# Kernel optimization log

Hardware: AMD Instinct MI355X
Metric: run time of the kernel (lower is better)

## Reference

```python
import jax, jax.numpy as jnp
import numpy as np

EPS = 1e-5
EXTEND_SCOPE = 1.0

def conv2d(x, w, b, pad):
    out = jax.lax.conv_general_dilated(x, w, (1, 1), [(pad, pad), (pad, pad)],
                                       dimension_numbers=('NCHW', 'OIHW', 'NCHW'))
    return out + b[None, :, None, None]

def group_norm(x, groups, gamma, beta):
    B, C, H, W = x.shape
    xg = x.reshape(B, groups, -1)
    mu = xg.mean(-1, keepdims=True)
    var = xg.var(-1, keepdims=True)
    xn = ((xg - mu) * jax.lax.rsqrt(var + EPS)).reshape(B, C, H, W)
    return xn * gamma[None, :, None, None] + beta[None, :, None, None]

def bilinear_sample(feat, y, x):
    # feat [B,C,H,W]; y,x pixel coords [B,Ho,Wo]; zeros padding, align_corners=True
    B, C, H, W = feat.shape
    flat = feat.reshape(B, C, H * W)
    y0 = jnp.floor(y); x0 = jnp.floor(x)
    wy = (y - y0)[:, None]; wx = (x - x0)[:, None]  # [B,1,Ho,Wo]
    y0i = y0.astype(jnp.int32); x0i = x0.astype(jnp.int32)
    Ho, Wo = y.shape[1], y.shape[2]
    def gather(yi, xi):
        valid = ((yi >= 0) & (yi < H) & (xi >= 0) & (xi < W)).astype(feat.dtype)[:, None]
        idx = (jnp.clip(yi, 0, H - 1) * W + jnp.clip(xi, 0, W - 1)).reshape(B, -1)
        g = jax.vmap(lambda f, i: f[:, i])(flat, idx).reshape(B, C, Ho, Wo)
        return g * valid
    g00 = gather(y0i, x0i)
    g01 = gather(y0i, x0i + 1)
    g10 = gather(y0i + 1, x0i)
    g11 = gather(y0i + 1, x0i + 1)
    return g00 * (1 - wy) * (1 - wx) + g01 * (1 - wy) * wx + g10 * wy * (1 - wx) + g11 * wy * wx

def setup_inputs() -> dict:
    key = jax.random.key(0)
    ks = jax.random.split(key, 4)
    B, C, H, W, K, O = 4, 64, 128, 128, 9, 64
    return {
        'x': jax.random.normal(ks[0], (B, C, H, W), jnp.float32),
        'w_off': jax.random.normal(ks[1], (K, C, 3, 3), jnp.float32) * 0.05,
        'b_off': jnp.zeros((K,), jnp.float32),
        'w_theta': jax.random.normal(ks[2], (K, C, 5, 5), jnp.float32) * 0.05,
        'b_theta': jnp.zeros((K,), jnp.float32),
        'gn_off_g': jnp.ones((K,), jnp.float32),
        'gn_off_b': jnp.zeros((K,), jnp.float32),
        'gn_th_g': jnp.ones((K,), jnp.float32),
        'gn_th_b': jnp.zeros((K,), jnp.float32),
        'w_strip': jax.random.normal(ks[3], (O, C, K, 1), jnp.float32) * 0.05,
        'b_strip': jnp.zeros((O,), jnp.float32),
        'gn_out_g': jnp.ones((O,), jnp.float32),
        'gn_out_b': jnp.zeros((O,), jnp.float32),
    }

def reference(x, w_off, b_off, w_theta, b_theta, gn_off_g, gn_off_b,
              gn_th_g, gn_th_b, w_strip, b_strip, gn_out_g, gn_out_b):
    B, C, H, W = x.shape
    K = w_off.shape[0]
    center = K // 2
    off = jnp.tanh(group_norm(conv2d(x, w_off, b_off, 1), 3, gn_off_g, gn_off_b))       # [B,K,H,W]
    th = jnp.arctan(group_norm(conv2d(x, w_theta, b_theta, 2), 3, gn_th_g, gn_th_b))    # [B,K,H,W]
    k = jnp.arange(K)
    s = (k - center).astype(x.dtype)[None, :, None, None]   # signed kernel offset
    m = center + jnp.abs(k - center)                        # mirror index (uses theta/offset at center+|i|)
    th_m = th[:, m]; off_m = off[:, m]                      # [B,K,H,W]
    is_center = (k == center)[None, :, None, None]
    y_off = jnp.where(is_center, 0.0, s * jnp.tan(th_m) + off_m * jnp.cos(th_m))
    x_off = jnp.where(is_center, 0.0, s - jnp.sin(th_m) * off_m)
    y_new = jnp.arange(H, dtype=x.dtype)[None, None, :, None] + s + EXTEND_SCOPE * y_off
    x_new = jnp.arange(W, dtype=x.dtype)[None, None, None, :] + s + EXTEND_SCOPE * x_off
    # rearrange 'b k h w -> b (h k) w'
    y_map = y_new.transpose(0, 2, 1, 3).reshape(B, H * K, W)
    x_map = x_new.transpose(0, 2, 1, 3).reshape(B, H * K, W)
    # clamp to valid range; scale to [-1,1] + align_corners=True grid_sample is identity in pixel space
    y_map = jnp.clip(y_map, 0.0, float(H - 1))
    x_map = jnp.clip(x_map, 0.0, float(W - 1))
    deformed = bilinear_sample(x, y_map, x_map)             # [B,C,K*H,W]
    d = deformed.reshape(B, C, H, K, W)
    out = jnp.einsum('bchkw,ock->bohw', d, w_strip[..., 0]) + b_strip[None, :, None, None]
    O = w_strip.shape[0]
    out = jax.nn.relu(group_norm(out, O // 4, gn_out_g, gn_out_b))
    return out
```

## Files before the change

kernel.cpp:

```cpp
#include <hip/hip_runtime.h>
#include <math.h>


typedef short v8s __attribute__((ext_vector_type(8)));
typedef float v4f __attribute__((ext_vector_type(4)));

__device__ __forceinline__ float fast_tanh(float a) {
    float aa = fabsf(a);
    float e = __expf(2.f * aa);
    float t = 1.f - 2.f / (e + 1.f);
    return copysignf(t, a);
}

__device__ __forceinline__ float bf2f(short s) {
    union { unsigned u; float f; } v;
    v.u = ((unsigned)(unsigned short)s) << 16;
    return v.f;
}

__global__ __launch_bounds__(256) void k_pack(
    const float* __restrict__ w_strip, short* __restrict__ w_pack)
{
    int idx = blockIdx.x * 256 + threadIdx.x;
    int j    = idx & 7;
    int lane = (idx >> 3) & 63;
    int kk   = (idx >> 9) & 1;
    int og   = (idx >> 10) & 3;
    int k    = idx >> 12;
    int c = (kk << 5) + ((lane >> 4) << 3) + j;
    int o = (og << 4) + (lane & 15);
    union { short s; __bf16 h; } u;
    u.h = (__bf16)w_strip[(o * 64 + c) * 9 + k];
    w_pack[idx] = u.s;
}

__global__ __launch_bounds__(256) void k_tr(
    const float* __restrict__ x, short* __restrict__ xt)
{
    __shared__ float l[64][65];
    const int t    = threadIdx.x;
    const int lane = t & 63;
    const int wv   = t >> 6;
    const int b    = blockIdx.x >> 8;
    const int pix0 = (blockIdx.x & 255) << 6;

#pragma unroll
    for (int it = 0; it < 16; ++it) {
        int c = (wv << 4) + it;
        l[lane][c] = x[(((size_t)(b << 6) + c) << 14) + pix0 + lane];
    }
    __syncthreads();
    {
        const int p   = t >> 2;
        const int c16 = (t & 3) << 4;
        union { v8s s8; __bf16 hh[8]; } u0, u1;
#pragma unroll
        for (int j = 0; j < 8; ++j) {
            u0.hh[j] = (__bf16)l[p][c16 + j];
            u1.hh[j] = (__bf16)l[p][c16 + 8 + j];
        }
        short* dst = xt + (((size_t)(b << 14) + pix0 + p) << 6) + c16;
        *(v8s*)dst = u0.s8;
        *(v8s*)(dst + 8) = u1.s8;
    }
}

__global__ __launch_bounds__(256, 8) void k_conv(
    const float* __restrict__ x,
    const float* __restrict__ w_off, const float* __restrict__ b_off,
    const float* __restrict__ w_th,  const float* __restrict__ b_th,
    float* __restrict__ off_raw, float* __restrict__ th_raw)
{
    __shared__ float tile[12][36];
    const int t  = threadIdx.x;
    const int tx = t & 31, ty = t >> 5;
    const int z  = blockIdx.z;
    const int b  = z >> 3, sp = z & 7;
    const int c0 = sp << 3;
    const int h0 = blockIdx.y << 3, w0 = blockIdx.x << 5;

    float accO[9], accT[9];
#pragma unroll
    for (int k = 0; k < 9; ++k) { accO[k] = 0.f; accT[k] = 0.f; }

    for (int ci = 0; ci < 8; ++ci) {
        const int c = c0 + ci;
        __syncthreads();
        const float* xp = x + (((size_t)(b << 6) + c) << 14);
        for (int e = t; e < 432; e += 256) {
            int r = e / 36, cc = e - r * 36;
            int hh = h0 + r - 2, ww = w0 + cc - 2;
            tile[r][cc] = (hh >= 0 && hh < 128 && ww >= 0 && ww < 128)
                            ? xp[(hh << 7) + ww] : 0.f;
        }
        __syncthreads();

        float win[5][5];
#pragma unroll
        for (int i = 0; i < 5; ++i)
#pragma unroll
            for (int j = 0; j < 5; ++j)
                win[i][j] = tile[ty + i][tx + j];

#pragma unroll
        for (int k = 0; k < 9; ++k) {
            const float* wo = w_off + (size_t)((k << 6) + c) * 9;
            float a = accO[k];
#pragma unroll
            for (int i = 0; i < 3; ++i)
#pragma unroll
                for (int j = 0; j < 3; ++j)
                    a = fmaf(win[i + 1][j + 1], wo[i * 3 + j], a);
            accO[k] = a;

            const float* wt = w_th + (size_t)((k << 6) + c) * 25;
            float bb = accT[k];
#pragma unroll
            for (int i = 0; i < 5; ++i)
#pragma unroll
                for (int j = 0; j < 5; ++j)
                    bb = fmaf(win[i][j], wt[i * 5 + j], bb);
            accT[k] = bb;
        }
    }

    const int pix = ((h0 + ty) << 7) + (w0 + tx);
#pragma unroll
    for (int k = 0; k < 9; ++k) {
        float vo = accO[k] + (sp == 0 ? b_off[k] : 0.f);
        float vt = accT[k] + (sp == 0 ? b_th[k]  : 0.f);
        atomicAdd(&off_raw[((b * 9 + k) << 14) + pix], vo);
        atomicAdd(&th_raw [((b * 9 + k) << 14) + pix], vt);
    }
}

__global__ __launch_bounds__(256) void k_stats(
    const float* __restrict__ off_raw, const float* __restrict__ th_raw,
    float* __restrict__ stats)
{
    const int id  = blockIdx.x;
    const int arr = id >= 36;
    const int rem = id - arr * 36;
    const float4* src = (const float4*)((arr ? th_raw : off_raw) + (rem << 14));

    float s1 = 0.f, s2 = 0.f;
    for (int i = threadIdx.x; i < 4096; i += 256) {
        float4 v = src[i];
        s1 += v.x + v.y + v.z + v.w;
        s2 += v.x * v.x + v.y * v.y + v.z * v.z + v.w * v.w;
    }
#pragma unroll
    for (int d = 32; d; d >>= 1) { s1 += __shfl_down(s1, d, 64); s2 += __shfl_down(s2, d, 64); }

    __shared__ float ls1[4], ls2[4];
    const int wv = threadIdx.x >> 6;
    if ((threadIdx.x & 63) == 0) { ls1[wv] = s1; ls2[wv] = s2; }
    __syncthreads();
    if (threadIdx.x == 0) {
        stats[arr * 72 + rem]      = ls1[0] + ls1[1] + ls1[2] + ls1[3];
        stats[arr * 72 + 36 + rem] = ls2[0] + ls2[1] + ls2[2] + ls2[3];
    }
}

__global__ __launch_bounds__(256, 4) void k_sample_strip3(
    const short* __restrict__ xt,
    const float* __restrict__ off_raw, const float* __restrict__ th_raw,
    const float* __restrict__ stats,
    const float* __restrict__ g_off, const float* __restrict__ be_off,
    const float* __restrict__ g_th,  const float* __restrict__ be_th,
    const short* __restrict__ w_pack, const float* __restrict__ b_strip,
    float* __restrict__ out, float* __restrict__ out_stats)
{
    __shared__ __align__(16) short smem[2][2048];
    const int t    = threadIdx.x;
    const int lane = t & 63;
    const int wv   = __builtin_amdgcn_readfirstlane(t >> 6);
    const int bid  = blockIdx.x;
    const int blk  = ((bid & 7) << 8) + (bid >> 3);
    const int b    = blk >> 9;
    const int pix0 = (blk & 511) << 5;
    const int l32  = lane & 31;
    const int q    = lane >> 5;
    const int p_img = pix0 + l32;
    const int h    = p_img >> 7, w = p_img & 127;
    const int i15  = lane & 15, lg = lane >> 4;
    const int cg   = (wv << 4) + (q << 3);
    const int cb   = (wv << 1) + q;

    const float inv_cnt = 1.f / (3.f * 16384.f);
    float muO1, isO1, muT1, isT1, muO2, isO2, muT2, isT2;
    {
        float s, qq, mu;
        s = stats[b*9+3] + stats[b*9+4] + stats[b*9+5];
        qq = stats[36+b*9+3] + stats[36+b*9+4] + stats[36+b*9+5];
        mu = s * inv_cnt; muO1 = mu;
        isO1 = rsqrtf(fmaxf(qq * inv_cnt - mu * mu, 0.f) + 1e-5f);
        s = stats[b*9+6] + stats[b*9+7] + stats[b*9+8];
        qq = stats[36+b*9+6] + stats[36+b*9+7] + stats[36+b*9+8];
        mu = s * inv_cnt; muO2 = mu;
        isO2 = rsqrtf(fmaxf(qq * inv_cnt - mu * mu, 0.f) + 1e-5f);
        s = stats[72+b*9+3] + stats[72+b*9+4] + stats[72+b*9+5];
        qq = stats[108+b*9+3] + stats[108+b*9+4] + stats[108+b*9+5];
        mu = s * inv_cnt; muT1 = mu;
        isT1 = rsqrtf(fmaxf(qq * inv_cnt - mu * mu, 0.f) + 1e-5f);
        s = stats[72+b*9+6] + stats[72+b*9+7] + stats[72+b*9+8];
        qq = stats[108+b*9+6] + stats[108+b*9+7] + stats[108+b*9+8];
        mu = s * inv_cnt; muT2 = mu;
        isT2 = rsqrtf(fmaxf(qq * inv_cnt - mu * mu, 0.f) + 1e-5f);
    }

    float zt[4], cyv[4], cxv[4];
#pragma unroll
    for (int m = 5; m <= 8; ++m) {
        const int mi = m - 5;
        float tv = th_raw [((b * 9 + m) << 14) + p_img];
        float ov = off_raw[((b * 9 + m) << 14) + p_img];
        float muT = (m == 5) ? muT1 : muT2, isT = (m == 5) ? isT1 : isT2;
        float muO = (m == 5) ? muO1 : muO2, isO = (m == 5) ? isO1 : isO2;
        float z = (tv - muT) * isT * g_th[m] + be_th[m];
        float f = fast_tanh((ov - muO) * isO * g_off[m] + be_off[m]);
        float r = rsqrtf(1.f + z * z);
        zt[mi]  = z;
        cyv[mi] = f * r;
        cxv[mi] = z * r * f;
    }

    const short* xtb = xt + ((size_t)b << 20);

    auto coords = [&](int k, float& cwy, float& cwx) -> int {
        float yy, xx;
        if (k == 4) { yy = (float)h; xx = (float)w; }
        else {
            const int s  = k - 4;
            const int mi = (s < 0 ? -s : s) - 1;
            const float fs = (float)s;
            yy = (float)h + fs + fs * zt[mi] + cyv[mi];
            xx = (float)w + 2.f * fs - cxv[mi];
            yy = fminf(fmaxf(yy, 0.f), 127.f);
            xx = fminf(fmaxf(xx, 0.f), 127.f);
        }
        int y0 = min((int)yy, 126), x0 = min((int)xx, 126);
        cwy = yy - (float)y0; cwx = xx - (float)x0;
        return (y0 << 7) + x0;
    };

    v8s G[4];
    v8s Af[2][2];
    float cwy, cwx, nwy, nwx;

    {
        int cidx = coords(0, cwy, cwx);
        const short* bb = xtb + ((size_t)cidx << 6) + cg;
        G[0] = *(const v8s*)bb;
        G[1] = *(const v8s*)(bb + 64);
        G[2] = *(const v8s*)(bb + 8192);
        G[3] = *(const v8s*)(bb + 8256);
        const short* wa = w_pack + ((0 * 4 + wv) << 10) + (lane << 3);
        Af[0][0] = *(const v8s*)wa;
        Af[0][1] = *(const v8s*)(wa + 512);
    }

    v4f acc[2];
    acc[0] = (v4f)0.f; acc[1] = (v4f)0.f;

#pragma unroll
    for (int k = 0; k < 9; ++k) {
        float vj[8];
#pragma unroll
        for (int j = 0; j < 8; ++j) {
            float c00 = bf2f(G[0][j]), c01 = bf2f(G[1][j]);
            float c10 = bf2f(G[2][j]), c11 = bf2f(G[3][j]);
            float top = fmaf(cwx, c01 - c00, c00);
            float bot = fmaf(cwx, c11 - c10, c10);
            vj[j] = fmaf(cwy, bot - top, top);
        }

        if (k < 8) {
            int cidx = coords(k + 1, nwy, nwx);
            const short* bb = xtb + ((size_t)cidx << 6) + cg;
            G[0] = *(const v8s*)bb;
            G[1] = *(const v8s*)(bb + 64);
            G[2] = *(const v8s*)(bb + 8192);
            G[3] = *(const v8s*)(bb + 8256);
            const short* wa = w_pack + ((((k + 1) << 2) + wv) << 10) + (lane << 3);
            Af[(k + 1) & 1][0] = *(const v8s*)wa;
            Af[(k + 1) & 1][1] = *(const v8s*)(wa + 512);
        }

        union { v8s s8; __bf16 hh[8]; } u;
#pragma unroll
        for (int j = 0; j < 8; ++j) u.hh[j] = (__bf16)vj[j];
        *(v8s*)&smem[k & 1][((cb << 5) + l32) << 3] = u.s8;

        __builtin_amdgcn_sched_barrier(0);
        asm volatile("s_waitcnt lgkmcnt(0)" ::: "memory");
        __builtin_amdgcn_s_barrier();
        __builtin_amdgcn_sched_barrier(0);

#pragma unroll
        for (int n = 0; n < 2; ++n) {
            int p16 = (n << 4) + i15;
            v8s b0 = *(const v8s*)&smem[k & 1][((lg << 5) + p16) << 3];
            v8s b1 = *(const v8s*)&smem[k & 1][(((lg + 4) << 5) + p16) << 3];
            acc[n] = __builtin_amdgcn_mfma_f32_16x16x32_bf16(Af[k & 1][0], b0, acc[n], 0, 0, 0);
            acc[n] = __builtin_amdgcn_mfma_f32_16x16x32_bf16(Af[k & 1][1], b1, acc[n], 0, 0, 0);
        }
        cwy = nwy; cwx = nwx;
    }

#pragma unroll
    for (int r = 0; r < 4; ++r) {
        int o = (wv << 4) + (lg << 2) + r;
        float bias = b_strip[o];
        float v0 = acc[0][r] + bias;
        float v1 = acc[1][r] + bias;
        float* op = out + (((size_t)(b << 6) + o) << 14) + pix0 + i15;
        op[0]  = v0;
        op[16] = v1;
        float s1 = v0 + v1;
        float s2 = v0 * v0 + v1 * v1;
#pragma unroll
        for (int d = 1; d <= 8; d <<= 1) {
            s1 += __shfl_xor(s1, d, 64);
            s2 += __shfl_xor(s2, d, 64);
        }
        if (i15 == 0) {
            atomicAdd(&out_stats[(b << 6) + o], s1);
            atomicAdd(&out_stats[256 + (b << 6) + o], s2);
        }
    }
}

__global__ __launch_bounds__(256) void k_sample_strip_old(
    const float* __restrict__ x,
    const float* __restrict__ off_raw, const float* __restrict__ th_raw,
    const float* __restrict__ stats,
    const float* __restrict__ g_off, const float* __restrict__ be_off,
    const float* __restrict__ g_th,  const float* __restrict__ be_th,
    const short* __restrict__ w_pack, const float* __restrict__ b_strip,
    float* __restrict__ out)
{
    __shared__ __align__(16) short smem[64 * 64];
    const int t    = threadIdx.x;
    const int lane = t & 63;
    const int wv   = __builtin_amdgcn_readfirstlane(t >> 6);
    const int bid  = blockIdx.x;
    const int blk  = ((bid & 7) << 7) + (bid >> 3);
    const int b    = blk >> 8;
    const int pix0 = (blk & 255) << 6;
    const int p    = pix0 + lane;
    const int h    = p >> 7, w = p & 127;
    const int i15  = lane & 15, lg = lane >> 4;

    float muO[3], isO[3], muT[3], isT[3];
    const float inv_cnt = 1.f / (3.f * 16384.f);
#pragma unroll
    for (int g = 0; g < 3; ++g) {
        float s = 0.f, q = 0.f;
#pragma unroll
        for (int j = 0; j < 3; ++j) { s += stats[b * 9 + 3 * g + j]; q += stats[36 + b * 9 + 3 * g + j]; }
        float mu = s * inv_cnt;
        muO[g] = mu; isO[g] = rsqrtf(fmaxf(q * inv_cnt - mu * mu, 0.f) + 1e-5f);
        s = 0.f; q = 0.f;
#pragma unroll
        for (int j = 0; j < 3; ++j) { s += stats[72 + b * 9 + 3 * g + j]; q += stats[108 + b * 9 + 3 * g + j]; }
        mu = s * inv_cnt;
        muT[g] = mu; isT[g] = rsqrtf(fmaxf(q * inv_cnt - mu * mu, 0.f) + 1e-5f);
    }

    const float* xb = x + ((size_t)((b << 6) + (wv << 4)) << 14);
    v4f acc[4];
#pragma unroll
    for (int n = 0; n < 4; ++n) acc[n] = (v4f)0.f;

    for (int k = 0; k < 9; ++k) {
        float v[16];
        if (k == 4) {
#pragma unroll
            for (int ci = 0; ci < 16; ++ci) v[ci] = xb[(ci << 14) + p];
        } else {
            const int s = k - 4;
            const int m = 4 + (s < 0 ? -s : s);
            const int g = m / 3;
            float z = (th_raw[((b * 9 + m) << 14) + p] - muT[g]) * isT[g] * g_th[m] + be_th[m];
            float f = fast_tanh((off_raw[((b * 9 + m) << 14) + p] - muO[g]) * isO[g] * g_off[m] + be_off[m]);
            float r = rsqrtf(1.f + z * z);
            float fs = (float)s;
            float yy = (float)h + fs + fs * z + f * r;
            float xx = (float)w + fs + fs - z * r * f;
            yy = fminf(fmaxf(yy, 0.f), 127.f);
            xx = fminf(fmaxf(xx, 0.f), 127.f);
            int y0 = min((int)yy, 126);
            int x0 = min((int)xx, 126);
            float wy = yy - (float)y0;
            float wx = xx - (float)x0;
            const float* base = xb + (y0 << 7) + x0;
#pragma unroll
            for (int ci = 0; ci < 16; ++ci) {
                const float* qp = base + (ci << 14);
                float2 r0 = *(const float2*)qp;
                float2 r1 = *(const float2*)(qp + 128);
                float lo = fmaf(wx, r0.y - r0.x, r0.x);
                float hi = fmaf(wx, r1.y - r1.x, r1.x);
                v[ci] = fmaf(wy, hi - lo, lo);
            }
        }

        union { v8s s8; __bf16 hh[8]; } u0, u1;
#pragma unroll
        for (int ci = 0; ci < 8; ++ci) { u0.hh[ci] = (__bf16)v[ci]; u1.hh[ci] = (__bf16)v[ci + 8]; }
        *(v8s*)&smem[(lane << 6) + ((((wv << 1) + 0) + lane) & 7) * 8] = u0.s8;
        *(v8s*)&smem[(lane << 6) + ((((wv << 1) + 1) + lane) & 7) * 8] = u1.s8;
        __syncthreads();

        const short* wpk = w_pack + (((k << 2) + wv) << 10) + (lane << 3);
        v8s a0 = *(const v8s*)wpk;
        v8s a1 = *(const v8s*)(wpk + 512);

#pragma unroll
        for (int n = 0; n < 4; ++n) {
            int r = (n << 4) + i15;
            v8s b0 = *(const v8s*)&smem[(r << 6) + (((lg    ) + r) & 7) * 8];
            v8s b1 = *(const v8s*)&smem[(r << 6) + (((lg + 4) + r) & 7) * 8];
            acc[n] = __builtin_amdgcn_mfma_f32_16x16x32_bf16(a0, b0, acc[n], 0, 0, 0);
            acc[n] = __builtin_amdgcn_mfma_f32_16x16x32_bf16(a1, b1, acc[n], 0, 0, 0);
        }
        __syncthreads();
    }

#pragma unroll
    for (int r = 0; r < 4; ++r) {
        int o = (wv << 4) + (lg << 2) + r;
        float bias = b_strip[o];
        float* op = out + ((size_t)((b << 6) + o) << 14) + pix0 + i15;
#pragma unroll
        for (int n = 0; n < 4; ++n)
            op[n << 4] = acc[n][r] + bias;
    }
}

__global__ __launch_bounds__(256) void k_stats_out(
    const float* __restrict__ out, float* __restrict__ out_stats)
{
    const int bo = blockIdx.x;
    const float4* src = (const float4*)(out + ((size_t)bo << 14));
    float s1 = 0.f, s2 = 0.f;
    for (int i = threadIdx.x; i < 4096; i += 256) {
        float4 v = src[i];
        s1 += v.x + v.y + v.z + v.w;
        s2 += v.x * v.x + v.y * v.y + v.z * v.z + v.w * v.w;
    }
#pragma unroll
    for (int d = 32; d; d >>= 1) { s1 += __shfl_down(s1, d, 64); s2 += __shfl_down(s2, d, 64); }

    __shared__ float ls1[4], ls2[4];
    const int wv = threadIdx.x >> 6;
    if ((threadIdx.x & 63) == 0) { ls1[wv] = s1; ls2[wv] = s2; }
    __syncthreads();
    if (threadIdx.x == 0) {
        out_stats[bo]       = ls1[0] + ls1[1] + ls1[2] + ls1[3];
        out_stats[256 + bo] = ls2[0] + ls2[1] + ls2[2] + ls2[3];
    }
}

__global__ __launch_bounds__(256) void k_gn_out(
    float* __restrict__ out, const float* __restrict__ out_stats,
    const float* __restrict__ gg, const float* __restrict__ gb)
{
    const float inv_cnt = 1.f / (4.f * 16384.f);
    const int n4 = 1 << 20;
    for (int idx = blockIdx.x * 256 + threadIdx.x; idx < n4; idx += gridDim.x * 256) {
        int flat = idx << 2;
        int ch = (flat >> 14) & 63;
        int b  = flat >> 20;
        int cb = (b << 6) + ((ch >> 2) << 2);
        float s = out_stats[cb] + out_stats[cb + 1] + out_stats[cb + 2] + out_stats[cb + 3];
        float q = out_stats[256 + cb] + out_stats[256 + cb + 1] + out_stats[256 + cb + 2] + out_stats[256 + cb + 3];
        float mu   = s * inv_cnt;
        float istd = rsqrtf(fmaxf(q * inv_cnt - mu * mu, 0.f) + 1e-5f);
        float ga = gg[ch] * istd;
        float be = gb[ch] - mu * ga;
        float4 v = *reinterpret_cast<float4*>(out + flat);
        v.x = fmaxf(fmaf(v.x, ga, be), 0.f);
        v.y = fmaxf(fmaf(v.y, ga, be), 0.f);
        v.z = fmaxf(fmaf(v.z, ga, be), 0.f);
        v.w = fmaxf(fmaf(v.w, ga, be), 0.f);
        *reinterpret_cast<float4*>(out + flat) = v;
    }
}

extern "C" void kernel_launch(void* const* d_in, const int* in_sizes, int n_in,
                              void* d_out, int out_size, void* d_ws, size_t ws_size,
                              hipStream_t stream)
{
    const float* x       = (const float*)d_in[0];
    const float* w_off   = (const float*)d_in[1];
    const float* b_off   = (const float*)d_in[2];
    const float* w_th    = (const float*)d_in[3];
    const float* b_th    = (const float*)d_in[4];
    const float* g_off   = (const float*)d_in[5];
    const float* be_off  = (const float*)d_in[6];
    const float* g_th    = (const float*)d_in[7];
    const float* be_th   = (const float*)d_in[8];
    const float* w_strip = (const float*)d_in[9];
    const float* b_strip = (const float*)d_in[10];
    const float* gg      = (const float*)d_in[11];
    const float* gb      = (const float*)d_in[12];

    float* out       = (float*)d_out;
    float* ws        = (float*)d_ws;
    float* off_raw   = ws;
    float* th_raw    = ws + 589824;
    float* stats     = ws + 1179648;
    float* out_stats = ws + 1179792;
    short* w_pack    = (short*)(ws + 1180304);
    short* xt        = (short*)(ws + 1198736);

    const size_t need_full = (size_t)(1198736 + 2097152) * sizeof(float);
    const bool big = ws_size >= need_full;

    hipMemsetAsync(ws, 0, (size_t)1180304 * sizeof(float), stream);

    k_pack<<<144, 256, 0, stream>>>(w_strip, w_pack);
    if (big) k_tr<<<1024, 256, 0, stream>>>(x, xt);
    dim3 g1(4, 16, 32);
    k_conv<<<g1, 256, 0, stream>>>(x, w_off, b_off, w_th, b_th, off_raw, th_raw);
    k_stats<<<72, 256, 0, stream>>>(off_raw, th_raw, stats);
    if (big) {
        k_sample_strip3<<<2048, 256, 0, stream>>>(xt, off_raw, th_raw, stats,
                                                  g_off, be_off, g_th, be_th,
                                                  w_pack, b_strip, out, out_stats);
    } else {
        k_sample_strip_old<<<1024, 256, 0, stream>>>(x, off_raw, th_raw, stats,
                                                     g_off, be_off, g_th, be_th,
                                                     w_pack, b_strip, out);
        k_stats_out<<<256, 256, 0, stream>>>(out, out_stats);
    }
    k_gn_out<<<4096, 256, 0, stream>>>(out, out_stats, gg, gb);
}
```

Baseline: 189.1 us.

## Prefetch conv input tiles into registers and deepen gather pipeline in sampler

```diff
diff --git a/kernel.cpp b/kernel.cpp
--- a/kernel.cpp
+++ b/kernel.cpp
@@ -65,7 +65,7 @@
     }
 }
 
-__global__ __launch_bounds__(256, 8) void k_conv(
+__global__ __launch_bounds__(256, 4) void k_conv(
     const float* __restrict__ x,
     const float* __restrict__ w_off, const float* __restrict__ b_off,
     const float* __restrict__ w_th,  const float* __restrict__ b_th,
@@ -75,25 +75,48 @@
     const int t  = threadIdx.x;
     const int tx = t & 31, ty = t >> 5;
     const int z  = blockIdx.z;
-    const int b  = z >> 3, sp = z & 7;
-    const int c0 = sp << 3;
+    const int b  = z >> 2, sp = z & 3;
+    const int c0 = sp << 4;
     const int h0 = blockIdx.y << 3, w0 = blockIdx.x << 5;
 
+    const int r1 = t / 36,        cc1 = t - r1 * 36;
+    const int e2 = t + 256;
+    const int r2 = e2 / 36,       cc2 = e2 - r2 * 36;
+    const int hh1 = h0 + r1 - 2,  ww1 = w0 + cc1 - 2;
+    const int hh2 = h0 + r2 - 2,  ww2 = w0 + cc2 - 2;
+    const bool va1 = (hh1 >= 0 && hh1 < 128 && ww1 >= 0 && ww1 < 128);
+    const bool va2 = (t < 176) && (hh2 >= 0 && hh2 < 128 && ww2 >= 0 && ww2 < 128);
+    const int of1 = (hh1 << 7) + ww1;
+    const int of2 = (hh2 << 7) + ww2;
+    const float* xb = x + (((size_t)(b << 6) + c0) << 14);
+
     float accO[9], accT[9];
 #pragma unroll
     for (int k = 0; k < 9; ++k) { accO[k] = 0.f; accT[k] = 0.f; }
 
-    for (int ci = 0; ci < 8; ++ci) {
+    float ra = va1 ? xb[of1] : 0.f;
+    float rb = va2 ? xb[of2] : 0.f;
+
+    for (int ci = 0; ci < 16; ++ci) {
         const int c = c0 + ci;
-        __syncthreads();
-        const float* xp = x + (((size_t)(b << 6) + c) << 14);
-        for (int e = t; e < 432; e += 256) {
-            int r = e / 36, cc = e - r * 36;
-            int hh = h0 + r - 2, ww = w0 + cc - 2;
-            tile[r][cc] = (hh >= 0 && hh < 128 && ww >= 0 && ww < 128)
-                            ? xp[(hh << 7) + ww] : 0.f;
-        }
-        __syncthreads();
+        __builtin_amdgcn_sched_barrier(0);
+        asm volatile("s_waitcnt lgkmcnt(0)" ::: "memory");
+        __builtin_amdgcn_s_barrier();
+        __builtin_amdgcn_sched_barrier(0);
+
+        tile[r1][cc1] = ra;
+        if (t < 176) tile[r2][cc2] = rb;
+
+        if (ci < 15) {
+            const float* xp = xb + ((size_t)(ci + 1) << 14);
+            ra = va1 ? xp[of1] : 0.f;
+            rb = va2 ? xp[of2] : 0.f;
+        }
+
+        __builtin_amdgcn_sched_barrier(0);
+        asm volatile("s_waitcnt lgkmcnt(0)" ::: "memory");
+        __builtin_amdgcn_s_barrier();
+        __builtin_amdgcn_sched_barrier(0);
 
         float win[5][5];
 #pragma unroll
@@ -228,37 +251,43 @@
     const short* xtb = xt + ((size_t)b << 20);
 
     auto coords = [&](int k, float& cwy, float& cwx) -> int {
-        float yy, xx;
-        if (k == 4) { yy = (float)h; xx = (float)w; }
-        else {
-            const int s  = k - 4;
-            const int mi = (s < 0 ? -s : s) - 1;
-            const float fs = (float)s;
-            yy = (float)h + fs + fs * zt[mi] + cyv[mi];
-            xx = (float)w + 2.f * fs - cxv[mi];
-            yy = fminf(fmaxf(yy, 0.f), 127.f);
-            xx = fminf(fmaxf(xx, 0.f), 127.f);
-        }
+        const int s  = k - 4;
+        const int mi = (s < 0 ? -s : s) - 1;
+        const float fs = (float)s;
+        float yy = (float)h + fs + fs * zt[mi] + cyv[mi];
+        float xx = (float)w + 2.f * fs - cxv[mi];
+        yy = fminf(fmaxf(yy, 0.f), 127.f);
+        xx = fminf(fmaxf(xx, 0.f), 127.f);
         int y0 = min((int)yy, 126), x0 = min((int)xx, 126);
         cwy = yy - (float)y0; cwx = xx - (float)x0;
         return (y0 << 7) + x0;
     };
 
-    v8s G[4];
+    v8s Gb[2][4];
     v8s Af[2][2];
-    float cwy, cwx, nwy, nwx;
-
-    {
-        int cidx = coords(0, cwy, cwx);
-        const short* bb = xtb + ((size_t)cidx << 6) + cg;
-        G[0] = *(const v8s*)bb;
-        G[1] = *(const v8s*)(bb + 64);
-        G[2] = *(const v8s*)(bb + 8192);
-        G[3] = *(const v8s*)(bb + 8256);
-        const short* wa = w_pack + ((0 * 4 + wv) << 10) + (lane << 3);
-        Af[0][0] = *(const v8s*)wa;
-        Af[0][1] = *(const v8s*)(wa + 512);
-    }
+    float wyv[2], wxv[2];
+
+    auto issueG = [&](int k) {
+        if (k == 4) {
+            const short* bb = xtb + ((size_t)p_img << 6) + cg;
+            Gb[k & 1][0] = *(const v8s*)bb;
+        } else {
+            int cidx = coords(k, wyv[k & 1], wxv[k & 1]);
+            const short* bb = xtb + ((size_t)cidx << 6) + cg;
+            Gb[k & 1][0] = *(const v8s*)bb;
+            Gb[k & 1][1] = *(const v8s*)(bb + 64);
+            Gb[k & 1][2] = *(const v8s*)(bb + 8192);
+            Gb[k & 1][3] = *(const v8s*)(bb + 8256);
+        }
+    };
+    auto issueA = [&](int k) {
+        const short* wa = w_pack + (((k << 2) + wv) << 10) + (lane << 3);
+        Af[k & 1][0] = *(const v8s*)wa;
+        Af[k & 1][1] = *(const v8s*)(wa + 512);
+    };
+
+    issueG(0); issueA(0);
+    issueG(1); issueA(1);
 
     v4f acc[2];
     acc[0] = (v4f)0.f; acc[1] = (v4f)0.f;
@@ -266,26 +295,22 @@
 #pragma unroll
     for (int k = 0; k < 9; ++k) {
         float vj[8];
-#pragma unroll
-        for (int j = 0; j < 8; ++j) {
-            float c00 = bf2f(G[0][j]), c01 = bf2f(G[1][j]);
-            float c10 = bf2f(G[2][j]), c11 = bf2f(G[3][j]);
-            float top = fmaf(cwx, c01 - c00, c00);
-            float bot = fmaf(cwx, c11 - c10, c10);
-            vj[j] = fmaf(cwy, bot - top, top);
-        }
-
-        if (k < 8) {
-            int cidx = coords(k + 1, nwy, nwx);
-            const short* bb = xtb + ((size_t)cidx << 6) + cg;
-            G[0] = *(const v8s*)bb;
-            G[1] = *(const v8s*)(bb + 64);
-            G[2] = *(const v8s*)(bb + 8192);
-            G[3] = *(const v8s*)(bb + 8256);
-            const short* wa = w_pack + ((((k + 1) << 2) + wv) << 10) + (lane << 3);
-            Af[(k + 1) & 1][0] = *(const v8s*)wa;
-            Af[(k + 1) & 1][1] = *(const v8s*)(wa + 512);
-        }
+        if (k == 4) {
+#pragma unroll
+            for (int j = 0; j < 8; ++j) vj[j] = bf2f(Gb[k & 1][0][j]);
+        } else {
+            const float cwy = wyv[k & 1], cwx = wxv[k & 1];
+#pragma unroll
+            for (int j = 0; j < 8; ++j) {
+                float c00 = bf2f(Gb[k & 1][0][j]), c01 = bf2f(Gb[k & 1][1][j]);
+                float c10 = bf2f(Gb[k & 1][2][j]), c11 = bf2f(Gb[k & 1][3][j]);
+                float top = fmaf(cwx, c01 - c00, c00);
+                float bot = fmaf(cwx, c11 - c10, c10);
+                vj[j] = fmaf(cwy, bot - top, top);
+            }
+        }
+
+        if (k < 7) issueG(k + 2);
 
         union { v8s s8; __bf16 hh[8]; } u;
 #pragma unroll
@@ -305,7 +330,8 @@
             acc[n] = __builtin_amdgcn_mfma_f32_16x16x32_bf16(Af[k & 1][0], b0, acc[n], 0, 0, 0);
             acc[n] = __builtin_amdgcn_mfma_f32_16x16x32_bf16(Af[k & 1][1], b1, acc[n], 0, 0, 0);
         }
-        cwy = nwy; cwx = nwx;
+
+        if (k < 7) issueA(k + 2);
     }
 
 #pragma unroll
@@ -523,7 +549,7 @@
 
     k_pack<<<144, 256, 0, stream>>>(w_strip, w_pack);
     if (big) k_tr<<<1024, 256, 0, stream>>>(x, xt);
-    dim3 g1(4, 16, 32);
+    dim3 g1(4, 16, 16);
     k_conv<<<g1, 256, 0, stream>>>(x, w_off, b_off, w_th, b_th, off_raw, th_raw);
     k_stats<<<72, 256, 0, stream>>>(off_raw, th_raw, stats);
     if (big) {
```

Result: faster. 174.9 us (-7.5%).
